# Performance work log

Measured on AMD Instinct MI355X. Metric: run time of the kernel, lower is better.

Reference implementation:

```python
import jax, jax.numpy as jnp
import numpy as np

VOCAB = 50257  # nn.Embedding num_embeddings (vocab)
H = 128        # hidden_size
L = 20         # num_layers
T = 1024       # seq_len (time-major, batch_first=False)
B = 128        # batch


def setup_inputs() -> dict:
    key = jax.random.key(0)
    ks = jax.random.split(key, 6)
    s = 1.0 / np.sqrt(H)  # PyTorch LSTM init range
    return {
        "x": jax.random.randint(ks[0], (T, B), 0, VOCAB, dtype=jnp.int32),
        "emb": jax.random.normal(ks[1], (VOCAB, H), jnp.float32) * 0.02,
        "W_ih": jax.random.uniform(ks[2], (L, 4 * H, H), jnp.float32, -s, s),
        "W_hh": jax.random.uniform(ks[3], (L, 4 * H, H), jnp.float32, -s, s),
        "b_ih": jax.random.uniform(ks[4], (L, 4 * H), jnp.float32, -s, s),
        "b_hh": jax.random.uniform(ks[5], (L, 4 * H), jnp.float32, -s, s),
    }


def _lstm_layer(inp, Wih, Whh, b):
    # inp: [T, B, H]; PyTorch gate order: i, f, g, o
    h0 = jnp.zeros((inp.shape[1], H), inp.dtype)
    c0 = h0

    def step(carry, xt):
        h, c = carry
        pre = xt @ Wih.T + h @ Whh.T + b  # [B, 4H]
        i, f, g, o = jnp.split(pre, 4, axis=-1)
        c = jax.nn.sigmoid(f) * c + jax.nn.sigmoid(i) * jnp.tanh(g)
        h = jax.nn.sigmoid(o) * jnp.tanh(c)
        return (h, c), h

    _, hs = jax.lax.scan(step, (h0, c0), inp)
    return hs  # [T, B, H]


def reference(x, emb, W_ih, W_hh, b_ih, b_hh):
    embedded = emb[x]  # [T, B, H] embedding lookup
    out = embedded
    for l in range(L):  # stacked layers (structural loop, not a data dim)
        out = _lstm_layer(out, W_ih[l], W_hh[l], b_ih[l] + b_hh[l])
    return (out, embedded)
```

## Files before the change

### kernel.cpp

```cpp
#include <hip/hip_runtime.h>

#define T_ 1024
#define B_ 128
#define H_ 128
#define L_ 20
#define G4H_ 512
#define NCH 8
#define RING 64
#define GRPSZ 2
#define FSTRIDE 32
#define LEAD 12

typedef _Float16 f16x8 __attribute__((ext_vector_type(8)));
typedef _Float16 f16x4 __attribute__((ext_vector_type(4)));
typedef float f32x4 __attribute__((ext_vector_type(4)));

__device__ __forceinline__ float fast_sig(float x) {
  float e = __builtin_amdgcn_exp2f(-1.44269504f * x);
  return __builtin_amdgcn_rcpf(1.0f + e);
}
__device__ __forceinline__ float fast_tanh(float x) {
  float e = __builtin_amdgcn_exp2f(2.88539008f * x);
  return 1.0f - 2.0f * __builtin_amdgcn_rcpf(e + 1.0f);
}

#define VMW(n) asm volatile("s_waitcnt vmcnt(" #n ")" ::: "memory")
#define LGKM0() asm volatile("s_waitcnt lgkmcnt(0)" ::: "memory")

__device__ __forceinline__ int flag_ld(const int* p) {
  int r;
  asm volatile("global_load_dword %0, %1, off sc1\n\ts_waitcnt vmcnt(0)"
               : "=v"(r) : "v"(p) : "memory");
  return r;
}
__device__ __forceinline__ void flag_issue(int* d, const int* p) {
  asm volatile("global_load_dword %0, %1, off sc1" : "=&v"(*d) : "v"(p) : "memory");
}
__device__ __forceinline__ void flag_st(int* p, int v) {
  asm volatile("global_store_dword %0, %1, off sc1" :: "v"(p), "v"(v) : "memory");
}
__device__ __forceinline__ void xld_sc1(f16x4* d, const _Float16* p) {
  asm volatile("global_load_dwordx2 %0, %1, off sc1" : "=&v"(*d) : "v"(p) : "memory");
}
__device__ __forceinline__ void xld_plain(f16x4* d, const _Float16* p) {
  asm volatile("global_load_dwordx2 %0, %1, off" : "=&v"(*d) : "v"(p) : "memory");
}
__device__ __forceinline__ void st8_sc1(_Float16* p, f16x4 v) {
  asm volatile("global_store_dwordx2 %0, %1, off sc1" :: "v"(p), "v"(v) : "memory");
}
__device__ __forceinline__ void st16_plain(float* p, f32x4 v) {
  asm volatile("global_store_dwordx4 %0, %1, off" :: "v"(p), "v"(v) : "memory");
}

__global__ void wconv_kernel(const float* __restrict__ Wih, const float* __restrict__ Whh,
                             _Float16* __restrict__ Wif, _Float16* __restrict__ Whf) {
  int i = blockIdx.x * 256 + threadIdx.x;
  if (i < L_ * G4H_ * H_) {
    Wif[i] = (_Float16)Wih[i];
    Whf[i] = (_Float16)Whh[i];
  }
}

__global__ void emb_kernel(const int* __restrict__ xids, const float* __restrict__ emb,
                           float* __restrict__ out_emb, _Float16* __restrict__ X0) {
  int row = blockIdx.x;
  int d = threadIdx.x;
  int tok = xids[row];
  float v = emb[(size_t)tok * H_ + d];
  out_emb[(size_t)row * H_ + d] = v;
  X0[(size_t)row * H_ + d] = (_Float16)v;
}

__launch_bounds__(512, 2)
__global__ void lstm_persist_kernel(const _Float16* __restrict__ Wif,
                                    const _Float16* __restrict__ Whf,
                                    const float* __restrict__ bih,
                                    const float* __restrict__ bhh,
                                    const _Float16* __restrict__ X0,
                                    _Float16* __restrict__ XR,
                                    float* __restrict__ out_h,
                                    int* __restrict__ rdy) {
  const int l = blockIdx.x >> 3;
  const int chunk = blockIdx.x & 7;
  const int tid = threadIdx.x;
  const int lane = tid & 63;
  const int wave = tid >> 6;
  const int lr = lane & 15;
  const int lhi = lane >> 4;
  const int ub = wave * 16;

  f16x8 wi[4][4], wh[4][4];
  f32x4 bias4[4];
  {
    const _Float16* wip = Wif + (size_t)l * G4H_ * H_;
    const _Float16* whp = Whf + (size_t)l * G4H_ * H_;
#pragma unroll
    for (int G = 0; G < 4; ++G) {
      int j = G * 128 + ub + lr;
#pragma unroll
      for (int kt = 0; kt < 4; ++kt) {
        wi[G][kt] = *(const f16x8*)(wip + (size_t)j * H_ + kt * 32 + lhi * 8);
        wh[G][kt] = *(const f16x8*)(whp + (size_t)j * H_ + kt * 32 + lhi * 8);
      }
      int jb = G * 128 + ub + lhi * 4;
      bias4[G] = *(const f32x4*)&bih[l * G4H_ + jb];
      bias4[G] += *(const f32x4*)&bhh[l * G4H_ + jb];
    }
  }

  __shared__ _Float16 xs[4][2048];
  __shared__ _Float16 hs[2][2048];

  const int xb = (tid >> 1) & 15;
  const int xk = ((tid >> 7) << 5) | (((tid >> 5) & 3) << 3) | ((tid & 1) << 2);
  const int hk = ub + lhi * 4;
  const int hdst = ((hk >> 5) << 9) + (((((hk & 31) >> 3) << 4) + lr) << 3) + ((lhi & 1) << 2);

  const size_t tile16 = (size_t)16 * H_;
  const _Float16* ring_in =
      (l > 0) ? XR + (size_t)((l - 1) * NCH + chunk) * RING * tile16 : X0;
  _Float16* ring_out = XR + (size_t)(l * NCH + chunk) * RING * tile16;

  int* rout = rdy + (l * NCH + chunk) * FSTRIDE;
  const int* rin = (l > 0) ? rdy + ((l - 1) * NCH + chunk) * FSTRIDE : rout;
  const int* rcons = (l < L_ - 1) ? rdy + ((l + 1) * NCH + chunk) * FSTRIDE : rout;

  auto xgsrc = [&](int t) -> const _Float16* {
    return (l == 0) ? X0 + ((size_t)t * B_ + chunk * 16 + xb) * H_ + xk
                    : ring_in + (size_t)(t & (RING - 1)) * tile16 + xb * H_ + xk;
  };

  int rin_c = 0, rcons_c = 0;
  int fR = 0, fC = 0;

  if (l > 0) {
    while (rin_c < LEAD) { rin_c = flag_ld(rin); __builtin_amdgcn_s_sleep(2); }
  }
  {
    f16x4 v0, v1, v2, v3;
    if (l == 0) { xld_plain(&v0, xgsrc(0)); xld_plain(&v1, xgsrc(1));
                  xld_plain(&v2, xgsrc(2)); xld_plain(&v3, xgsrc(3)); }
    else        { xld_sc1(&v0, xgsrc(0)); xld_sc1(&v1, xgsrc(1));
                  xld_sc1(&v2, xgsrc(2)); xld_sc1(&v3, xgsrc(3)); }
    VMW(0);
    *(f16x4*)&xs[0][tid * 4] = v0;
    *(f16x4*)&xs[1][tid * 4] = v1;
    *(f16x4*)&xs[2][tid * 4] = v2;
    *(f16x4*)&xs[3][tid * 4] = v3;
  }
  LGKM0();
  __builtin_amdgcn_s_barrier();

  float cst[4] = {0.f, 0.f, 0.f, 0.f};
  f32x4 a0[4], a1[4];
  {
    f16x8 xf[4];
#pragma unroll
    for (int kt = 0; kt < 4; ++kt) xf[kt] = *(const f16x8*)&xs[0][kt * 512 + lane * 8];
#pragma unroll
    for (int G = 0; G < 4; ++G) a0[G] = bias4[G];
#pragma unroll
    for (int kt = 0; kt < 4; ++kt)
#pragma unroll
      for (int G = 0; G < 4; ++G)
        a0[G] = __builtin_amdgcn_mfma_f32_16x16x32_f16(wi[G][kt], xf[kt], a0[G], 0, 0, 0);
  }

  f16x4 xspE, xspO;

#define STEP(t_, AC, AN, XSP, CVM, ODD)                                          \
  {                                                                              \
    const int t = (t_);                                                          \
    if (t > 0) {                                                \
      f16x8 hf[4];                                                               \
      _Pragma("unroll")                                                          \
      for (int kt = 0; kt < 4; ++kt)                                             \
        hf[kt] = *(const f16x8*)&hs[(t - 1) & 1][kt * 512 + lane * 8];           \
      _Pragma("unroll")                                                          \
      for (int kt = 0; kt < 4; ++kt)                                             \
        _Pragma("unroll")                                                        \
        for (int G = 0; G < 4; ++G)                                              \
          AC[G] = __builtin_amdgcn_mfma_f32_16x16x32_f16(wh[G][kt], hf[kt], AC[G], 0, 0, 0); \
    }                                                                            \
    if (t + 1 < T_) {                                  \
      f16x8 xf[4];                                                               \
      _Pragma("unroll")                                                          \
      for (int kt = 0; kt < 4; ++kt)                                             \
        xf[kt] = *(const f16x8*)&xs[(t + 1) & 3][kt * 512 + lane * 8];           \
      _Pragma("unroll")                                                          \
      for (int G = 0; G < 4; ++G) AN[G] = bias4[G];                              \
      _Pragma("unroll")                                                          \
      for (int kt = 0; kt < 4; ++kt)                                             \
        _Pragma("unroll")                                                        \
        for (int G = 0; G < 4; ++G)                                              \
          AN[G] = __builtin_amdgcn_mfma_f32_16x16x32_f16(wi[G][kt], xf[kt], AN[G], 0, 0, 0); \
    }                                                                            \
    if (t >= 2 && t + 2 < T_) {                     \
      if (t >= T_ - 8) { VMW(0); } else { VMW(CVM); }                            \
      *(f16x4*)&xs[(t + 2) & 3][tid * 4] = XSP;                                  \
    }                                                                            \
    float hnew[4];                                                    \
    _Pragma("unroll")                                                            \
    for (int r = 0; r < 4; ++r) {                                                \
      float iv = fast_sig(AC[0][r]);                                             \
      float fv = fast_sig(AC[1][r]);                                             \
      float gv = fast_tanh(AC[2][r]);                                            \
      float ov = fast_sig(AC[3][r]);                                             \
      float c = fv * cst[r] + iv * gv;                                           \
      cst[r] = c;                                                                \
      hnew[r] = ov * fast_tanh(c);                                               \
    }                                                                            \
    if (l < L_ - 1) {                       \
      f16x4 hp;                                                                  \
      _Pragma("unroll")                                                          \
      for (int r = 0; r < 4; ++r) hp[r] = (_Float16)hnew[r];                     \
      st8_sc1(ring_out + (size_t)(t & (RING - 1)) * tile16 + lr * H_ + hk, hp);  \
      *(f16x4*)&hs[t & 1][hdst] = hp;                                            \
    } else {                                           \
      f32x4 ov4;                                                                 \
      _Pragma("unroll")                                                          \
      for (int r = 0; r < 4; ++r) ov4[r] = hnew[r];                              \
      st16_plain(out_h + ((size_t)t * B_ + chunk * 16 + lr) * H_ + hk, ov4);     \
      f16x4 hp;                                                                  \
      _Pragma("unroll")                                                          \
      for (int r = 0; r < 4; ++r) hp[r] = (_Float16)hnew[r];                     \
      *(f16x4*)&hs[t & 1][hdst] = hp;                                            \
    }                                                                            \
    if (!(ODD)) {            \
      flag_issue(&fR, (int*)rin);                                                \
      flag_issue(&fC, (int*)rcons);                                              \
    }                                                                            \
    if (t + 4 < T_) {                                       \
      if (l == 0) xld_plain(&XSP, xgsrc(t + 4)); else xld_sc1(&XSP, xgsrc(t + 4)); \
    }                                                                            \
    if (ODD) { if (t >= T_ - 8) { VMW(0); } else { VMW(1); } }                   \
    LGKM0();                                                                     \
    __builtin_amdgcn_s_barrier();                                                \
  }

  for (int tg = 0; tg < T_; tg += GRPSZ) {
    if (tg > 0) {
      if (lane == 0) flag_st(rout, tg);
      rin_c = fR > rin_c ? fR : rin_c;
      rcons_c = fC > rcons_c ? fC : rcons_c;
      if (l > 0) {
        int need = tg + 3 * GRPSZ; if (need > T_) need = T_;
        while (rin_c < need) { rin_c = flag_ld(rin); __builtin_amdgcn_s_sleep(2); }
      }
      if (l < L_ - 1) {
        int need = tg + GRPSZ - RING + 8;
        if (need > 0)
          while (rcons_c < need) { rcons_c = flag_ld(rcons); __builtin_amdgcn_s_sleep(2); }
      }
    }
    STEP(tg, a0, a1, xspE, 2, 0)
    STEP(tg + 1, a1, a0, xspO, 5, 1)
  }

  __syncthreads();
  if (tid == 0) flag_st(rout, T_);
}

extern "C" void kernel_launch(void* const* d_in, const int* in_sizes, int n_in,
                              void* d_out, int out_size, void* d_ws, size_t ws_size,
                              hipStream_t stream) {
  const int* xids = (const int*)d_in[0];
  const float* emb = (const float*)d_in[1];
  const float* Wih = (const float*)d_in[2];
  const float* Whh = (const float*)d_in[3];
  const float* bih = (const float*)d_in[4];
  const float* bhh = (const float*)d_in[5];
  float* out = (float*)d_out;
  float* out_h = out;
  float* out_emb = out + (size_t)T_ * B_ * H_;

  char* ws = (char*)d_ws;
  const size_t RDY_BYTES = (size_t)L_ * NCH * FSTRIDE * 4;
  const size_t X0_BYTES = (size_t)T_ * B_ * H_ * 2;
  const size_t XR_BYTES = (size_t)L_ * NCH * RING * 16 * H_ * 2;
  const size_t WF_BYTES = (size_t)L_ * G4H_ * H_ * 2;
  int* rdyp = (int*)ws;
  _Float16* X0 = (_Float16*)(ws + RDY_BYTES);
  _Float16* XR = (_Float16*)(ws + RDY_BYTES + X0_BYTES);
  _Float16* Wif = (_Float16*)(ws + RDY_BYTES + X0_BYTES + XR_BYTES);
  _Float16* Whf = (_Float16*)(ws + RDY_BYTES + X0_BYTES + XR_BYTES + WF_BYTES);

  hipMemsetAsync(rdyp, 0, RDY_BYTES, stream);
  wconv_kernel<<<(L_ * G4H_ * H_ + 255) / 256, 256, 0, stream>>>(Wih, Whh, Wif, Whf);
  emb_kernel<<<T_ * B_, H_, 0, stream>>>(xids, emb, out_emb, X0);

  void* args[] = {(void*)&Wif, (void*)&Whf, (void*)&bih, (void*)&bhh,
                  (void*)&X0,  (void*)&XR,  (void*)&out_h, (void*)&rdyp};
  hipLaunchCooperativeKernel((void*)lstm_persist_kernel, dim3(L_ * NCH), dim3(512),
                             args, 0, stream);
}
```

Baseline: 1.730 ms.

## Store inter-layer activations in MFMA fragment layout and load directly into registers

Embedding output and inter-layer ring buffers are now written in the MFMA B-operand fragment layout, so each wave loads its x fragments with 16-byte global loads straight into registers. This removes the LDS staging buffer for x and its per-step store and barrier traffic. Flag publishing and polling are grouped every 4 steps instead of 2, which cuts synchronisation overhead but adds latency between layers in the wavefront pipeline. Each wave now loads the full x tile redundantly from global or L2 memory.

```diff
diff --git a/kernel.cpp b/kernel.cpp
--- a/kernel.cpp
+++ b/kernel.cpp
@@ -7,7 +7,7 @@
 #define G4H_ 512
 #define NCH 8
 #define RING 64
-#define GRPSZ 2
+#define GRP 4
 #define FSTRIDE 32
 #define LEAD 12
 
@@ -39,11 +39,11 @@
 __device__ __forceinline__ void flag_st(int* p, int v) {
   asm volatile("global_store_dword %0, %1, off sc1" :: "v"(p), "v"(v) : "memory");
 }
-__device__ __forceinline__ void xld_sc1(f16x4* d, const _Float16* p) {
-  asm volatile("global_load_dwordx2 %0, %1, off sc1" : "=&v"(*d) : "v"(p) : "memory");
-}
-__device__ __forceinline__ void xld_plain(f16x4* d, const _Float16* p) {
-  asm volatile("global_load_dwordx2 %0, %1, off" : "=&v"(*d) : "v"(p) : "memory");
+__device__ __forceinline__ void ld16_sc1(f16x8* d, const _Float16* p) {
+  asm volatile("global_load_dwordx4 %0, %1, off sc1" : "=&v"(*d) : "v"(p) : "memory");
+}
+__device__ __forceinline__ void ld16_plain(f16x8* d, const _Float16* p) {
+  asm volatile("global_load_dwordx4 %0, %1, off" : "=&v"(*d) : "v"(p) : "memory");
 }
 __device__ __forceinline__ void st8_sc1(_Float16* p, f16x4 v) {
   asm volatile("global_store_dwordx2 %0, %1, off sc1" :: "v"(p), "v"(v) : "memory");
@@ -65,10 +65,12 @@
                            float* __restrict__ out_emb, _Float16* __restrict__ X0) {
   int row = blockIdx.x;
   int d = threadIdx.x;
+  int t = row >> 7, b = row & 127;
   int tok = xids[row];
   float v = emb[(size_t)tok * H_ + d];
   out_emb[(size_t)row * H_ + d] = v;
-  X0[(size_t)row * H_ + d] = (_Float16)v;
+  int fidx = ((d >> 5) << 9) | (((((d >> 3) & 3) << 4) | (b & 15)) << 3) | (d & 7);
+  X0[((size_t)t * NCH + (b >> 4)) * 2048 + fidx] = (_Float16)v;
 }
 
 __launch_bounds__(512, 2)
@@ -88,6 +90,8 @@
   const int lr = lane & 15;
   const int lhi = lane >> 4;
   const int ub = wave * 16;
+  const int hk = ub + lhi * 4;
+  const int hdst = ((hk >> 5) << 9) + (((((hk >> 3) & 3) << 4) + lr) << 3) + ((lhi & 1) << 2);
 
   f16x8 wi[4][4], wh[4][4];
   f32x4 bias4[4];
@@ -108,153 +112,131 @@
     }
   }
 
-  __shared__ _Float16 xs[4][2048];
-  __shared__ _Float16 hs[2][2048];
-
-  const int xb = (tid >> 1) & 15;
-  const int xk = ((tid >> 7) << 5) | (((tid >> 5) & 3) << 3) | ((tid & 1) << 2);
-  const int hk = ub + lhi * 4;
-  const int hdst = ((hk >> 5) << 9) + (((((hk & 31) >> 3) << 4) + lr) << 3) + ((lhi & 1) << 2);
-
-  const size_t tile16 = (size_t)16 * H_;
+  __shared__ __align__(16) _Float16 hs[2][2048];
+
   const _Float16* ring_in =
-      (l > 0) ? XR + (size_t)((l - 1) * NCH + chunk) * RING * tile16 : X0;
-  _Float16* ring_out = XR + (size_t)(l * NCH + chunk) * RING * tile16;
+      (l > 0) ? XR + (size_t)((l - 1) * NCH + chunk) * (RING * 2048) : (const _Float16*)0;
+  _Float16* ring_out = XR + (size_t)(l * NCH + chunk) * (RING * 2048);
 
   int* rout = rdy + (l * NCH + chunk) * FSTRIDE;
   const int* rin = (l > 0) ? rdy + ((l - 1) * NCH + chunk) * FSTRIDE : rout;
   const int* rcons = (l < L_ - 1) ? rdy + ((l + 1) * NCH + chunk) * FSTRIDE : rout;
 
-  auto xgsrc = [&](int t) -> const _Float16* {
-    return (l == 0) ? X0 + ((size_t)t * B_ + chunk * 16 + xb) * H_ + xk
-                    : ring_in + (size_t)(t & (RING - 1)) * tile16 + xb * H_ + xk;
-  };
-
-  int rin_c = 0, rcons_c = 0;
+  f16x8 xf[4];
   int fR = 0, fC = 0;
 
+#define XISSUE(t_) {                                                              \
+    if (l == 0) {                                                                 \
+      const _Float16* bp = X0 + ((size_t)(t_) * NCH + chunk) * 2048 + lane * 8;   \
+      ld16_plain(&xf[0], bp);       ld16_plain(&xf[1], bp + 512);                 \
+      ld16_plain(&xf[2], bp + 1024); ld16_plain(&xf[3], bp + 1536);               \
+    } else {                                                                      \
+      const _Float16* bp = ring_in + (size_t)((t_) & (RING - 1)) * 2048 + lane * 8; \
+      ld16_sc1(&xf[0], bp);       ld16_sc1(&xf[1], bp + 512);                     \
+      ld16_sc1(&xf[2], bp + 1024); ld16_sc1(&xf[3], bp + 1536);                   \
+    } }
+
   if (l > 0) {
-    while (rin_c < LEAD) { rin_c = flag_ld(rin); __builtin_amdgcn_s_sleep(2); }
-  }
-  {
-    f16x4 v0, v1, v2, v3;
-    if (l == 0) { xld_plain(&v0, xgsrc(0)); xld_plain(&v1, xgsrc(1));
-                  xld_plain(&v2, xgsrc(2)); xld_plain(&v3, xgsrc(3)); }
-    else        { xld_sc1(&v0, xgsrc(0)); xld_sc1(&v1, xgsrc(1));
-                  xld_sc1(&v2, xgsrc(2)); xld_sc1(&v3, xgsrc(3)); }
-    VMW(0);
-    *(f16x4*)&xs[0][tid * 4] = v0;
-    *(f16x4*)&xs[1][tid * 4] = v1;
-    *(f16x4*)&xs[2][tid * 4] = v2;
-    *(f16x4*)&xs[3][tid * 4] = v3;
-  }
-  LGKM0();
-  __builtin_amdgcn_s_barrier();
-
+    int v = 0;
+    while ((v = flag_ld(rin)) < LEAD) __builtin_amdgcn_s_sleep(2);
+    fR = v;
+  }
   float cst[4] = {0.f, 0.f, 0.f, 0.f};
   f32x4 a0[4], a1[4];
-  {
-    f16x8 xf[4];
-#pragma unroll
-    for (int kt = 0; kt < 4; ++kt) xf[kt] = *(const f16x8*)&xs[0][kt * 512 + lane * 8];
-#pragma unroll
-    for (int G = 0; G < 4; ++G) a0[G] = bias4[G];
-#pragma unroll
-    for (int kt = 0; kt < 4; ++kt)
-#pragma unroll
-      for (int G = 0; G < 4; ++G)
-        a0[G] = __builtin_amdgcn_mfma_f32_16x16x32_f16(wi[G][kt], xf[kt], a0[G], 0, 0, 0);
-  }
-
-  f16x4 xspE, xspO;
-
-#define STEP(t_, AC, AN, XSP, CVM, ODD)                                          \
-  {                                                                              \
-    const int t = (t_);                                                          \
-    if (t > 0) {                                                \
-      f16x8 hf[4];                                                               \
-      _Pragma("unroll")                                                          \
-      for (int kt = 0; kt < 4; ++kt)                                             \
-        hf[kt] = *(const f16x8*)&hs[(t - 1) & 1][kt * 512 + lane * 8];           \
-      _Pragma("unroll")                                                          \
-      for (int kt = 0; kt < 4; ++kt)                                             \
-        _Pragma("unroll")                                                        \
-        for (int G = 0; G < 4; ++G)                                              \
-          AC[G] = __builtin_amdgcn_mfma_f32_16x16x32_f16(wh[G][kt], hf[kt], AC[G], 0, 0, 0); \
-    }                                                                            \
-    if (t + 1 < T_) {                                  \
-      f16x8 xf[4];                                                               \
-      _Pragma("unroll")                                                          \
-      for (int kt = 0; kt < 4; ++kt)                                             \
-        xf[kt] = *(const f16x8*)&xs[(t + 1) & 3][kt * 512 + lane * 8];           \
-      _Pragma("unroll")                                                          \
-      for (int G = 0; G < 4; ++G) AN[G] = bias4[G];                              \
-      _Pragma("unroll")                                                          \
-      for (int kt = 0; kt < 4; ++kt)                                             \
-        _Pragma("unroll")                                                        \
-        for (int G = 0; G < 4; ++G)                                              \
+  XISSUE(0);
+  VMW(0);
+  __builtin_amdgcn_sched_barrier(0);
+#pragma unroll
+  for (int G = 0; G < 4; ++G) a0[G] = bias4[G];
+#pragma unroll
+  for (int kt = 0; kt < 4; ++kt)
+#pragma unroll
+    for (int G = 0; G < 4; ++G)
+      a0[G] = __builtin_amdgcn_mfma_f32_16x16x32_f16(wi[G][kt], xf[kt], a0[G], 0, 0, 0);
+  XISSUE(1);
+  flag_issue(&fR, rin);
+  flag_issue(&fC, rcons);
+
+#define STEP(t_, AC, AN, VMN) {                                                   \
+    const int t = (t_);                                                           \
+    if (t > 0) {          \
+      f16x8 hf0 = *(const f16x8*)&hs[(t - 1) & 1][lane * 8];                      \
+      f16x8 hf1 = *(const f16x8*)&hs[(t - 1) & 1][512 + lane * 8];                \
+      f16x8 hf2 = *(const f16x8*)&hs[(t - 1) & 1][1024 + lane * 8];               \
+      f16x8 hf3 = *(const f16x8*)&hs[(t - 1) & 1][1536 + lane * 8];               \
+      _Pragma("unroll")                                                           \
+      for (int G = 0; G < 4; ++G) {                                               \
+        AC[G] = __builtin_amdgcn_mfma_f32_16x16x32_f16(wh[G][0], hf0, AC[G], 0, 0, 0); \
+        AC[G] = __builtin_amdgcn_mfma_f32_16x16x32_f16(wh[G][1], hf1, AC[G], 0, 0, 0); \
+        AC[G] = __builtin_amdgcn_mfma_f32_16x16x32_f16(wh[G][2], hf2, AC[G], 0, 0, 0); \
+        AC[G] = __builtin_amdgcn_mfma_f32_16x16x32_f16(wh[G][3], hf3, AC[G], 0, 0, 0); \
+      }                                                                           \
+    }                                                                             \
+    if (t + 1 < T_) {                        \
+      VMW(VMN);                                                                   \
+      __builtin_amdgcn_sched_barrier(0);                                          \
+      _Pragma("unroll")                                                           \
+      for (int G = 0; G < 4; ++G) AN[G] = bias4[G];                               \
+      _Pragma("unroll")                                                           \
+      for (int kt = 0; kt < 4; ++kt)                                              \
+        _Pragma("unroll")                                                         \
+        for (int G = 0; G < 4; ++G)                                               \
           AN[G] = __builtin_amdgcn_mfma_f32_16x16x32_f16(wi[G][kt], xf[kt], AN[G], 0, 0, 0); \
-    }                                                                            \
-    if (t >= 2 && t + 2 < T_) {                     \
-      if (t >= T_ - 8) { VMW(0); } else { VMW(CVM); }                            \
-      *(f16x4*)&xs[(t + 2) & 3][tid * 4] = XSP;                                  \
-    }                                                                            \
-    float hnew[4];                                                    \
-    _Pragma("unroll")                                                            \
-    for (int r = 0; r < 4; ++r) {                                                \
-      float iv = fast_sig(AC[0][r]);                                             \
-      float fv = fast_sig(AC[1][r]);                                             \
-      float gv = fast_tanh(AC[2][r]);                                            \
-      float ov = fast_sig(AC[3][r]);                                             \
-      float c = fv * cst[r] + iv * gv;                                           \
-      cst[r] = c;                                                                \
-      hnew[r] = ov * fast_tanh(c);                                               \
-    }                                                                            \
-    if (l < L_ - 1) {                       \
-      f16x4 hp;                                                                  \
-      _Pragma("unroll")                                                          \
-      for (int r = 0; r < 4; ++r) hp[r] = (_Float16)hnew[r];                     \
-      st8_sc1(ring_out + (size_t)(t & (RING - 1)) * tile16 + lr * H_ + hk, hp);  \
-      *(f16x4*)&hs[t & 1][hdst] = hp;                                            \
-    } else {                                           \
-      f32x4 ov4;                                                                 \
-      _Pragma("unroll")                                                          \
-      for (int r = 0; r < 4; ++r) ov4[r] = hnew[r];                              \
-      st16_plain(out_h + ((size_t)t * B_ + chunk * 16 + lr) * H_ + hk, ov4);     \
-      f16x4 hp;                                                                  \
-      _Pragma("unroll")                                                          \
-      for (int r = 0; r < 4; ++r) hp[r] = (_Float16)hnew[r];                     \
-      *(f16x4*)&hs[t & 1][hdst] = hp;                                            \
-    }                                                                            \
-    if (!(ODD)) {            \
-      flag_issue(&fR, (int*)rin);                                                \
-      flag_issue(&fC, (int*)rcons);                                              \
-    }                                                                            \
-    if (t + 4 < T_) {                                       \
-      if (l == 0) xld_plain(&XSP, xgsrc(t + 4)); else xld_sc1(&XSP, xgsrc(t + 4)); \
-    }                                                                            \
-    if (ODD) { if (t >= T_ - 8) { VMW(0); } else { VMW(1); } }                   \
-    LGKM0();                                                                     \
-    __builtin_amdgcn_s_barrier();                                                \
-  }
-
-  for (int tg = 0; tg < T_; tg += GRPSZ) {
-    if (tg > 0) {
-      if (lane == 0) flag_st(rout, tg);
-      rin_c = fR > rin_c ? fR : rin_c;
-      rcons_c = fC > rcons_c ? fC : rcons_c;
-      if (l > 0) {
-        int need = tg + 3 * GRPSZ; if (need > T_) need = T_;
-        while (rin_c < need) { rin_c = flag_ld(rin); __builtin_amdgcn_s_sleep(2); }
-      }
-      if (l < L_ - 1) {
-        int need = tg + GRPSZ - RING + 8;
-        if (need > 0)
-          while (rcons_c < need) { rcons_c = flag_ld(rcons); __builtin_amdgcn_s_sleep(2); }
-      }
+    }                                                                             \
+    if (t + 2 < T_) XISSUE(t + 2);           \
+    float hnew[4];                                                                \
+    _Pragma("unroll")                                                             \
+    for (int r = 0; r < 4; ++r) {                                                 \
+      float iv = fast_sig(AC[0][r]);                                              \
+      float fv = fast_sig(AC[1][r]);                                              \
+      float gv = fast_tanh(AC[2][r]);                                             \
+      float ov = fast_sig(AC[3][r]);                                              \
+      float c = fv * cst[r] + iv * gv;                                            \
+      cst[r] = c;                                                                 \
+      hnew[r] = ov * fast_tanh(c);                                                \
+    }                                                                             \
+    f16x4 hp;                                                                     \
+    _Pragma("unroll")                                                             \
+    for (int r = 0; r < 4; ++r) hp[r] = (_Float16)hnew[r];                        \
+    if (l < L_ - 1) {           \
+      st8_sc1(ring_out + (size_t)(t & (RING - 1)) * 2048 + hdst, hp);             \
+    } else {                                          \
+      f32x4 ov4;                                                                  \
+      _Pragma("unroll")                                                           \
+      for (int r = 0; r < 4; ++r) ov4[r] = hnew[r];                               \
+      st16_plain(out_h + ((size_t)t * B_ + chunk * 16 + lr) * H_ + hk, ov4);      \
+    }                                                                             \
+    *(f16x4*)&hs[t & 1][hdst] = hp;                                               \
+    LGKM0();                                                                      \
+    __builtin_amdgcn_s_barrier();                                                 \
+    asm volatile("" ::: "memory");                                                \
+  }
+
+  STEP(0, a0, a1, 2)
+  STEP(1, a1, a0, 1)
+  STEP(2, a0, a1, 1)
+  STEP(3, a1, a0, 1)
+
+  for (int tg = GRP; tg < T_; tg += GRP) {
+    VMW(0);
+    __builtin_amdgcn_s_barrier();
+    asm volatile("" ::: "memory");
+    if (tid == 0) flag_st(rout, tg);
+    if (l > 0) {
+      int need = tg + GRP + 2; if (need > T_) need = T_;
+      while (fR < need) { fR = flag_ld(rin); __builtin_amdgcn_s_sleep(2); }
     }
-    STEP(tg, a0, a1, xspE, 2, 0)
-    STEP(tg + 1, a1, a0, xspO, 5, 1)
+    if (l < L_ - 1) {
+      int need = tg - 52;
+      if (need > 0)
+        while (fC < need) { fC = flag_ld(rcons); __builtin_amdgcn_s_sleep(2); }
+    }
+    flag_issue(&fR, rin);
+    flag_issue(&fC, rcons);
+    STEP(tg, a0, a1, 3)
+    STEP(tg + 1, a1, a0, 1)
+    STEP(tg + 2, a0, a1, 1)
+    STEP(tg + 3, a1, a0, 1)
   }
 
   __syncthreads();
@@ -277,7 +259,7 @@
   char* ws = (char*)d_ws;
   const size_t RDY_BYTES = (size_t)L_ * NCH * FSTRIDE * 4;
   const size_t X0_BYTES = (size_t)T_ * B_ * H_ * 2;
-  const size_t XR_BYTES = (size_t)L_ * NCH * RING * 16 * H_ * 2;
+  const size_t XR_BYTES = (size_t)L_ * NCH * RING * 2048 * 2;
   const size_t WF_BYTES = (size_t)L_ * G4H_ * H_ * 2;
   int* rdyp = (int*)ws;
   _Float16* X0 = (_Float16*)(ws + RDY_BYTES);
```

After: 1.444 ms. -16.5%, faster.
